# Optimization experiments

Hardware: AMD Instinct MI355X
Metric: run time of the kernel (lower is better)

Reference implementation:

```python
import jax, jax.numpy as jnp
import numpy as np
from jax import lax

STRIDE = 4
RADII = (0.1, 0.2)
NSAMPLES = (16, 32)


def fps(xyz, npoint):
    """Iterative farthest point sampling. xyz: (B,N,3) -> idx (B,npoint) int32."""
    B, N, _ = xyz.shape

    def body(carry, _):
        dists, last = carry  # (B,N), (B,)
        last_pt = jnp.take_along_axis(xyz, last[:, None, None], axis=1)  # (B,1,3)
        d = jnp.sum((xyz - last_pt) ** 2, axis=-1)  # (B,N)
        dists = jnp.minimum(dists, d)
        nxt = jnp.argmax(dists, axis=-1).astype(jnp.int32)
        return (dists, nxt), last

    init = (jnp.full((B, N), 1e10, xyz.dtype), jnp.zeros((B,), jnp.int32))
    _, idxs = lax.scan(body, init, None, length=npoint)
    return jnp.transpose(idxs)  # (B, npoint)


def ball_query(radius, nsample, support_xyz, query_xyz):
    """First-nsample-in-ball neighbor indices, padded with the first valid index.
    Returns idx (B,S,K) int32."""
    N = support_xyz.shape[1]
    d2 = (jnp.sum(query_xyz ** 2, -1, keepdims=True)
          + jnp.sum(support_xyz ** 2, -1)[:, None, :]
          - 2.0 * jnp.einsum('bsd,bnd->bsn', query_xyz, support_xyz))  # (B,S,N)
    in_ball = d2 <= radius * radius
    key = jnp.where(in_ball, jnp.arange(N, dtype=jnp.int32), N)  # smallest index first
    neg_key, idx = lax.top_k(-key, nsample)  # smallest keys
    valid = (-neg_key) < N
    idx = jnp.where(valid, idx, idx[..., :1])  # pad empty slots with first neighbor
    return idx


def gather_points(pts, idx):
    """pts (B,N,D), idx (B,S,K) -> (B,S,K,D)"""
    B, S, K = idx.shape
    D = pts.shape[-1]
    out = jnp.take_along_axis(pts, idx.reshape(B, S * K, 1), axis=1)
    return out.reshape(B, S, K, D)


def scale_block(query_xyz, support_xyz, feats_t, radius, nsample, weights):
    idx = ball_query(radius, nsample, support_xyz, query_xyz)
    g_xyz = gather_points(support_xyz, idx) - query_xyz[:, :, None, :]  # relative coords
    g_feat = gather_points(feats_t, idx)
    h = jnp.concatenate([g_xyz, g_feat], axis=-1)  # (B,S,K,3+C)
    for W, b in weights:  # shared pointwise MLP (1x1 conv) + ReLU
        h = jax.nn.relu(jnp.einsum('bskc,cd->bskd', h, W) + b)
    return jnp.max(h, axis=2)  # max-pool over neighbors -> (B,S,Cout)


def setup_inputs() -> dict:
    key = jax.random.key(0)
    ks = jax.random.split(key, 10)
    B, N, C = 8, 8192, 64
    inp = {
        'support_xyz': jax.random.uniform(ks[0], (B, N, 3), jnp.float32),
        'support_features': jax.random.normal(ks[1], (B, C, N), jnp.float32),
    }
    dims0 = [(67, 64), (64, 64), (64, 128)]
    dims1 = [(67, 64), (64, 96), (96, 128)]
    k = 2
    for s, dims in ((0, dims0), (1, dims1)):
        for j, (din, dout) in enumerate(dims):
            inp[f's{s}_w{j}'] = jax.random.normal(ks[k], (din, dout), jnp.float32) * 0.02
            inp[f's{s}_b{j}'] = jnp.zeros((dout,), jnp.float32)
            k += 1
    return inp


def reference(support_xyz, support_features,
              s0_w0, s0_b0, s0_w1, s0_b1, s0_w2, s0_b2,
              s1_w0, s1_b0, s1_w1, s1_b1, s1_w2, s1_b2):
    B, N, _ = support_xyz.shape
    npoint = N // STRIDE
    idx = fps(support_xyz, npoint)  # (B,npoint)
    query_xyz = jnp.take_along_axis(support_xyz, idx[:, :, None], axis=1)  # (B,npoint,3)
    feats_t = jnp.transpose(support_features, (0, 2, 1))  # (B,N,C)
    w0 = [(s0_w0, s0_b0), (s0_w1, s0_b1), (s0_w2, s0_b2)]
    w1 = [(s1_w0, s1_b0), (s1_w1, s1_b1), (s1_w2, s1_b2)]
    f0 = scale_block(query_xyz, support_xyz, feats_t, RADII[0], NSAMPLES[0], w0)
    f1 = scale_block(query_xyz, support_xyz, feats_t, RADII[1], NSAMPLES[1], w1)
    new_features = jnp.transpose(jnp.concatenate([f0, f1], axis=-1), (0, 2, 1))  # (B,256,npoint)
    return query_xyz, new_features
```

## Files before the change

### kernel.cpp

```cpp
#include <hip/hip_runtime.h>

#define N_SUP 8192
#define N_QPT 2048

typedef float v2f __attribute__((ext_vector_type(2)));

__device__ __forceinline__ float sumsq3(float x, float y, float z) {
#pragma clang fp contract(off)
  return x * x + y * y + z * z;
}

__device__ __forceinline__ float dot3(float ax, float ay, float az,
                                      float bx, float by, float bz) {
#pragma clang fp contract(off)
  return ax * bx + ay * by + az * bz;
}

__device__ __forceinline__ float d2_expand(float A, float Bn, float d) {
#pragma clang fp contract(off)
  return (A + Bn) - 2.0f * d;
}

template <int CTRL>
__device__ __forceinline__ float dppmax(float m) {
  int mi = __float_as_int(m);
  int mv = __builtin_amdgcn_update_dpp(mi, mi, CTRL, 0xf, 0xf, false);
  return fmaxf(m, __int_as_float(mv));
}

__device__ __forceinline__ float wavemax_dpp(float m) {
  m = dppmax<0x111>(m);
  m = dppmax<0x112>(m);
  m = dppmax<0x114>(m);
  m = dppmax<0x118>(m);
  m = dppmax<0x142>(m);
  m = dppmax<0x143>(m);
  return m;
}

template <int CTRL>
__device__ __forceinline__ unsigned dppminu(unsigned m) {
  unsigned mv = (unsigned)__builtin_amdgcn_update_dpp((int)m, (int)m, CTRL,
                                                      0xf, 0xf, false);
  return (mv < m) ? mv : m;
}

__device__ __forceinline__ unsigned wavemin_dpp(unsigned m) {
  m = dppminu<0x111>(m);
  m = dppminu<0x112>(m);
  m = dppminu<0x114>(m);
  m = dppminu<0x118>(m);
  m = dppminu<0x142>(m);
  m = dppminu<0x143>(m);
  return m;
}

__global__ __launch_bounds__(256) void prep_xyz_kernel(
    const float* __restrict__ xyz, float* __restrict__ xs,
    float* __restrict__ ys, float* __restrict__ zs, float* __restrict__ bsq) {
  int p = blockIdx.x * 256 + threadIdx.x;
  float x = xyz[p * 3 + 0];
  float y = xyz[p * 3 + 1];
  float z = xyz[p * 3 + 2];
  xs[p] = x; ys[p] = y; zs[p] = z;
  bsq[p] = sumsq3(x, y, z);
}

__global__ __launch_bounds__(256) void transpose_feats_kernel(
    const float* __restrict__ feats, float* __restrict__ fT) {
  __shared__ float tile[64][65];
  int b = blockIdx.x >> 7;
  int nb = (blockIdx.x & 127) << 6;
  int t = threadIdx.x;
#pragma unroll
  for (int i = 0; i < 16; ++i) {
    int e = i * 256 + t;
    int c = e >> 6, n = e & 63;
    tile[n][c] = feats[(b * 64 + c) * N_SUP + nb + n];
  }
  __syncthreads();
#pragma unroll
  for (int i = 0; i < 16; ++i) {
    int e = i * 256 + t;
    int n = e >> 6, c = e & 63;
    fT[(b * N_SUP + nb + n) * 64 + c] = tile[n][c];
  }
}

__global__ __launch_bounds__(512, 1) void fps_kernel(
    const float* __restrict__ xs, const float* __restrict__ ys,
    const float* __restrict__ zs, float* __restrict__ qxyz) {
  const int b = blockIdx.x;
  const int t = threadIdx.x;
  __shared__ float sx[N_SUP], sy[N_SUP], sz[N_SUP];
  __shared__ __align__(16) unsigned long long skey[2][8];
  const float* bx = xs + b * N_SUP;
  const float* by = ys + b * N_SUP;
  const float* bz = zs + b * N_SUP;
  v2f px[8], py[8], pz[8], dm[8];
#pragma unroll
  for (int j = 0; j < 8; ++j) {
    int n0 = t + (2 * j) * 512, n1 = t + (2 * j + 1) * 512;
    float x0 = bx[n0], x1 = bx[n1];
    float y0 = by[n0], y1 = by[n1];
    float z0 = bz[n0], z1 = bz[n1];
    px[j] = (v2f){x0, x1}; py[j] = (v2f){y0, y1}; pz[j] = (v2f){z0, z1};
    sx[n0] = x0; sx[n1] = x1;
    sy[n0] = y0; sy[n1] = y1;
    sz[n0] = z0; sz[n1] = z1;
    dm[j] = (v2f){1e10f, 1e10f};
  }
  float lx = bx[0], ly = by[0], lz = bz[0];
  float* q = qxyz + b * N_QPT * 3;
  if (t == 0) { q[0] = lx; q[1] = ly; q[2] = lz; }
  const int wv = t >> 6;
  const bool is63 = (t & 63) == 63;
  for (int it = 1; it < N_QPT; ++it) {
    float nx = -lx, ny = -ly, nz = -lz;
    v2f nx2 = (v2f){nx, nx}, ny2 = (v2f){ny, ny}, nz2 = (v2f){nz, nz};
    float lm = -1.0f;
#pragma unroll
    for (int j = 0; j < 8; ++j) {
#pragma clang fp contract(off)
      v2f dx = px[j] + nx2;
      v2f dy = py[j] + ny2;
      v2f dz = pz[j] + nz2;
      v2f s = dx * dx + dy * dy;
      s = s + dz * dz;
      v2f nd = __builtin_elementwise_min(dm[j], s);
      dm[j] = nd;
      lm = fmaxf(lm, fmaxf(nd.x, nd.y));
    }
    float wmx = wavemax_dpp(lm);
    float wm = __int_as_float(
        __builtin_amdgcn_readlane(__float_as_int(wmx), 63));
    int slot = 0x10000;
#pragma unroll
    for (int j = 7; j >= 0; --j) {
      if (dm[j].y == wm) slot = 2 * j + 1;
      if (dm[j].x == wm) slot = 2 * j;
    }
    unsigned li = (unsigned)(slot * 512 + t);
    unsigned wli = wavemin_dpp(li);
    if (is63) {
      skey[it & 1][wv] =
          (((unsigned long long)(unsigned)__float_as_int(wmx)) << 32) |
          (unsigned)(N_SUP - 1 - (int)wli);
    }
    __syncthreads();
    const ulonglong2* pk = (const ulonglong2*)&skey[it & 1][0];
    ulonglong2 A = pk[0], B = pk[1], C = pk[2], D = pk[3];
    unsigned long long k0 = (A.y > A.x) ? A.y : A.x;
    unsigned long long k1 = (B.y > B.x) ? B.y : B.x;
    unsigned long long k2 = (C.y > C.x) ? C.y : C.x;
    unsigned long long k3 = (D.y > D.x) ? D.y : D.x;
    k0 = (k1 > k0) ? k1 : k0;
    k2 = (k3 > k2) ? k3 : k2;
    k0 = (k2 > k0) ? k2 : k0;
    int ri = N_SUP - 1 - (int)(unsigned)(k0 & 0xFFFFFFFFull);
    lx = sx[ri]; ly = sy[ri]; lz = sz[ri];
    if (t == 0) { q[it * 3 + 0] = lx; q[it * 3 + 1] = ly; q[it * 3 + 2] = lz; }
  }
}

__global__ __launch_bounds__(256) void ballquery_kernel(
    const float* __restrict__ qxyz, const float* __restrict__ xs,
    const float* __restrict__ ys, const float* __restrict__ zs,
    const float* __restrict__ bsq, int* __restrict__ idx0,
    int* __restrict__ idx1) {
  const int lane = threadIdx.x & 63;
  const int qg = (blockIdx.x * 256 + threadIdx.x) >> 6;
  const int b = qg >> 11;
  const float qx = qxyz[qg * 3 + 0];
  const float qy = qxyz[qg * 3 + 1];
  const float qz = qxyz[qg * 3 + 2];
  const float A = sumsq3(qx, qy, qz);
  const float* sx = xs + b * N_SUP;
  const float* sy = ys + b * N_SUP;
  const float* sz = zs + b * N_SUP;
  const float* sq = bsq + b * N_SUP;
  int* o0 = idx0 + qg * 16;
  int* o1 = idx1 + qg * 32;
  int cnt0 = 0, cnt1 = 0, first0 = 0, first1 = 0;
  const unsigned long long ltmask = (1ull << lane) - 1ull;
  for (int base = 0; base < N_SUP; base += 64) {
    int n = base + lane;
    float d = dot3(qx, qy, qz, sx[n], sy[n], sz[n]);
    float d2 = d2_expand(A, sq[n], d);
    bool in1 = d2 <= 0.04f;
    bool in0 = d2 <= 0.01f;
    unsigned long long m1 = __ballot(in1);
    unsigned long long m0 = __ballot(in0);
    if (in1) {
      int pos = cnt1 + __popcll(m1 & ltmask);
      if (pos < 32) o1[pos] = n;
    }
    if (in0) {
      int pos = cnt0 + __popcll(m0 & ltmask);
      if (pos < 16) o0[pos] = n;
    }
    if (cnt1 == 0 && m1 != 0ull) first1 = base + __ffsll(m1) - 1;
    if (cnt0 == 0 && m0 != 0ull) first0 = base + __ffsll(m0) - 1;
    cnt1 += __popcll(m1);
    cnt0 += __popcll(m0);
    if (cnt0 >= 16 && cnt1 >= 32) break;
  }
  for (int p = cnt0 + lane; p < 16; p += 64) o0[p] = first0;
  for (int p = cnt1 + lane; p < 32; p += 64) o1[p] = first1;
}

template <int CIN, int SIN, int D, int SOUT>
__device__ __forceinline__ void dense_layer(const float* __restrict__ hin,
                                            float* __restrict__ hout,
                                            const float* __restrict__ W,
                                            const float* __restrict__ Bv,
                                            int w, int lane) {
  constexpr int CH = D / 16;
#pragma unroll
  for (int pass = 0; pass * 4 < CH; ++pass) {
    const int chunk = pass * 4 + w;
    if (chunk < CH) {
      const int co = chunk * 16;
      float acc[16];
#pragma unroll
      for (int j = 0; j < 16; ++j) acc[j] = Bv[co + j];
      const float* hr = hin + lane * SIN;
      const float* wp = W + co;
#pragma unroll 4
      for (int c = 0; c < CIN; ++c) {
        float a = hr[c];
#pragma unroll
        for (int j = 0; j < 16; ++j) acc[j] = fmaf(a, wp[c * D + j], acc[j]);
      }
      float* ho = hout + lane * SOUT + co;
#pragma unroll
      for (int j = 0; j < 16; ++j) ho[j] = fmaxf(acc[j], 0.0f);
    }
  }
}

template <int K, int Q, int C2, int S2, int CHOFF>
__global__ __launch_bounds__(256, 4) void mlp_kernel(
    const int* __restrict__ idxl, const float* __restrict__ qxyz,
    const float* __restrict__ xs, const float* __restrict__ ys,
    const float* __restrict__ zs, const float* __restrict__ fT,
    const float* __restrict__ W1, const float* __restrict__ B1,
    const float* __restrict__ W2, const float* __restrict__ B2,
    const float* __restrict__ W3, const float* __restrict__ B3,
    float* __restrict__ outf) {
  constexpr int S0 = 67, S1 = 65;
  constexpr int H0 = 64 * S0, H1 = 64 * S1, H2 = 64 * S2;
  constexpr int SM = H1 + (H2 > H0 ? H2 : H0);
  __shared__ float smem[SM];
  float* h1 = smem;
  float* h0 = smem + H1;
  float* h2 = smem + H1;
  const int t = threadIdx.x;
  const int w = __builtin_amdgcn_readfirstlane(t >> 6);
  const int lane = t & 63;
  for (int e = t; e < H0; e += 256) {
    int r = e / S0, c = e - r * S0;
    int qi = r / K, k = r - qi * K;
    int qg = blockIdx.x * Q + qi;
    int b = qg >> 11;
    int n = idxl[qg * K + k];
    float v;
    if (c < 3) {
      const float* sp = (c == 0) ? xs : (c == 1) ? ys : zs;
      v = sp[b * N_SUP + n] - qxyz[qg * 3 + c];
    } else {
      v = fT[(b * N_SUP + n) * 64 + (c - 3)];
    }
    h0[e] = v;
  }
  __syncthreads();
  dense_layer<67, S0, 64, S1>(h0, h1, W1, B1, w, lane);
  __syncthreads();
  dense_layer<64, S1, C2, S2>(h1, h2, W2, B2, w, lane);
  __syncthreads();
#pragma unroll
  for (int pass = 0; pass < 2; ++pass) {
    const int co = (pass * 4 + w) * 16;
    float acc[16];
#pragma unroll
    for (int j = 0; j < 16; ++j) acc[j] = B3[co + j];
    const float* hr = h2 + lane * S2;
#pragma unroll 4
    for (int c = 0; c < C2; ++c) {
      float a = hr[c];
#pragma unroll
      for (int j = 0; j < 16; ++j) acc[j] = fmaf(a, W3[c * 128 + co + j], acc[j]);
    }
#pragma unroll
    for (int j = 0; j < 16; ++j) acc[j] = fmaxf(acc[j], 0.0f);
#pragma unroll
    for (int off = K / 2; off >= 1; off >>= 1) {
#pragma unroll
      for (int j = 0; j < 16; ++j)
        acc[j] = fmaxf(acc[j], __shfl_xor(acc[j], off));
    }
    if ((lane & (K - 1)) == 0) {
      int qg = blockIdx.x * Q + (lane / K);
      int b = qg >> 11, s = qg & 2047;
      float* dst = outf + ((b * 256 + CHOFF + co) * 2048 + s);
#pragma unroll
      for (int j = 0; j < 16; ++j) dst[j * 2048] = acc[j];
    }
  }
}

extern "C" void kernel_launch(void* const* d_in, const int* in_sizes, int n_in,
                              void* d_out, int out_size, void* d_ws,
                              size_t ws_size, hipStream_t stream) {
  const float* xyz = (const float*)d_in[0];
  const float* feats = (const float*)d_in[1];
  const float* wt[12];
  for (int i = 0; i < 12; ++i) wt[i] = (const float*)d_in[2 + i];

  float* ws = (float*)d_ws;
  float* xs = ws;
  float* ys = ws + 65536;
  float* zs = ws + 131072;
  float* bsq = ws + 196608;
  float* fT = ws + 262144;
  int* idx0 = (int*)(ws + 4456448);
  int* idx1 = idx0 + 262144;

  float* qxyz = (float*)d_out;
  float* outf = qxyz + 8 * 2048 * 3;

  prep_xyz_kernel<<<dim3(256), dim3(256), 0, stream>>>(xyz, xs, ys, zs, bsq);
  transpose_feats_kernel<<<dim3(1024), dim3(256), 0, stream>>>(feats, fT);
  fps_kernel<<<dim3(8), dim3(512), 0, stream>>>(xs, ys, zs, qxyz);
  ballquery_kernel<<<dim3(4096), dim3(256), 0, stream>>>(qxyz, xs, ys, zs, bsq,
                                                         idx0, idx1);
  mlp_kernel<16, 4, 64, 65, 0><<<dim3(4096), dim3(256), 0, stream>>>(
      idx0, qxyz, xs, ys, zs, fT, wt[0], wt[1], wt[2], wt[3], wt[4], wt[5],
      outf);
  mlp_kernel<32, 2, 96, 97, 128><<<dim3(8192), dim3(256), 0, stream>>>(
      idx1, qxyz, xs, ys, zs, fT, wt[6], wt[7], wt[8], wt[9], wt[10], wt[11],
      outf);
}
```

Baseline: 2.823 ms.

## Spatially bin FPS points and skip threads whose bounding box cannot change

Points are counting-sorted into an 8x8x8 grid in shared memory so each thread owns 16 spatially coherent points with a bounding box. Each FPS iteration, a thread skips its distance update if the new sample is farther from its box than its current max distance, and whole waves skip the reduction when no lane is dirty. Argmax is reduced as a packed 64-bit key carrying the original index for tie-breaking. This adds a sort prologue, 64-bit DPP reductions, and depends on coordinates lying in [0,1) for the binning.

After: 2.893 ms. +2.5%, slower.

```diff
diff --git a/kernel.cpp b/kernel.cpp
--- a/kernel.cpp
+++ b/kernel.cpp
@@ -22,37 +22,24 @@
 }
 
 template <int CTRL>
-__device__ __forceinline__ float dppmax(float m) {
-  int mi = __float_as_int(m);
-  int mv = __builtin_amdgcn_update_dpp(mi, mi, CTRL, 0xf, 0xf, false);
-  return fmaxf(m, __int_as_float(mv));
-}
-
-__device__ __forceinline__ float wavemax_dpp(float m) {
-  m = dppmax<0x111>(m);
-  m = dppmax<0x112>(m);
-  m = dppmax<0x114>(m);
-  m = dppmax<0x118>(m);
-  m = dppmax<0x142>(m);
-  m = dppmax<0x143>(m);
-  return m;
-}
-
-template <int CTRL>
-__device__ __forceinline__ unsigned dppminu(unsigned m) {
-  unsigned mv = (unsigned)__builtin_amdgcn_update_dpp((int)m, (int)m, CTRL,
-                                                      0xf, 0xf, false);
-  return (mv < m) ? mv : m;
-}
-
-__device__ __forceinline__ unsigned wavemin_dpp(unsigned m) {
-  m = dppminu<0x111>(m);
-  m = dppminu<0x112>(m);
-  m = dppminu<0x114>(m);
-  m = dppminu<0x118>(m);
-  m = dppminu<0x142>(m);
-  m = dppminu<0x143>(m);
-  return m;
+__device__ __forceinline__ unsigned long long dppmax64(unsigned long long k) {
+  unsigned lo = (unsigned)k, hi = (unsigned)(k >> 32);
+  unsigned olo =
+      (unsigned)__builtin_amdgcn_update_dpp((int)lo, (int)lo, CTRL, 0xf, 0xf, false);
+  unsigned ohi =
+      (unsigned)__builtin_amdgcn_update_dpp((int)hi, (int)hi, CTRL, 0xf, 0xf, false);
+  unsigned long long o = (((unsigned long long)ohi) << 32) | olo;
+  return (o > k) ? o : k;
+}
+
+__device__ __forceinline__ unsigned long long wavemax_u64(unsigned long long k) {
+  k = dppmax64<0x111>(k);
+  k = dppmax64<0x112>(k);
+  k = dppmax64<0x114>(k);
+  k = dppmax64<0x118>(k);
+  k = dppmax64<0x142>(k);
+  k = dppmax64<0x143>(k);
+  return k;
 }
 
 __global__ __launch_bounds__(256) void prep_xyz_kernel(
@@ -93,60 +80,115 @@
   const int b = blockIdx.x;
   const int t = threadIdx.x;
   __shared__ float sx[N_SUP], sy[N_SUP], sz[N_SUP];
+  __shared__ unsigned short sorig[N_SUP];
+  __shared__ unsigned int hist[512], offs[512], cursor[512];
   __shared__ __align__(16) unsigned long long skey[2][8];
   const float* bx = xs + b * N_SUP;
   const float* by = ys + b * N_SUP;
   const float* bz = zs + b * N_SUP;
+
+  hist[t] = 0u;
+  __syncthreads();
+  for (int j = 0; j < 16; ++j) {
+    int n = t + j * 512;
+    float x = bx[n], y = by[n], z = bz[n];
+    int cx = min(7, (int)(x * 8.0f));
+    int cy = min(7, (int)(y * 8.0f));
+    int cz = min(7, (int)(z * 8.0f));
+    atomicAdd(&hist[(cx << 6) | (cy << 3) | cz], 1u);
+  }
+  __syncthreads();
+  offs[t] = hist[t];
+  __syncthreads();
+  for (int d = 1; d < 512; d <<= 1) {
+    unsigned v = (t >= d) ? offs[t - d] : 0u;
+    __syncthreads();
+    offs[t] += v;
+    __syncthreads();
+  }
+  cursor[t] = offs[t] - hist[t];
+  __syncthreads();
+  for (int j = 0; j < 16; ++j) {
+    int n = t + j * 512;
+    float x = bx[n], y = by[n], z = bz[n];
+    int cx = min(7, (int)(x * 8.0f));
+    int cy = min(7, (int)(y * 8.0f));
+    int cz = min(7, (int)(z * 8.0f));
+    unsigned pos = atomicAdd(&cursor[(cx << 6) | (cy << 3) | cz], 1u);
+    sx[pos] = x; sy[pos] = y; sz[pos] = z;
+    sorig[pos] = (unsigned short)n;
+  }
+  __syncthreads();
+
   v2f px[8], py[8], pz[8], dm[8];
+  unsigned payx[8], payy[8];
+  const int base = t * 16;
 #pragma unroll
   for (int j = 0; j < 8; ++j) {
-    int n0 = t + (2 * j) * 512, n1 = t + (2 * j + 1) * 512;
-    float x0 = bx[n0], x1 = bx[n1];
-    float y0 = by[n0], y1 = by[n1];
-    float z0 = bz[n0], z1 = bz[n1];
-    px[j] = (v2f){x0, x1}; py[j] = (v2f){y0, y1}; pz[j] = (v2f){z0, z1};
-    sx[n0] = x0; sx[n1] = x1;
-    sy[n0] = y0; sy[n1] = y1;
-    sz[n0] = z0; sz[n1] = z1;
+    int p0 = base + 2 * j, p1 = p0 + 1;
+    px[j] = (v2f){sx[p0], sx[p1]};
+    py[j] = (v2f){sy[p0], sy[p1]};
+    pz[j] = (v2f){sz[p0], sz[p1]};
+    payx[j] = ((unsigned)(N_SUP - 1 - sorig[p0]) << 13) | (unsigned)p0;
+    payy[j] = ((unsigned)(N_SUP - 1 - sorig[p1]) << 13) | (unsigned)p1;
     dm[j] = (v2f){1e10f, 1e10f};
   }
-  float lx = bx[0], ly = by[0], lz = bz[0];
+  float lox = px[0].x, hix = px[0].x;
+  float loy = py[0].x, hiy = py[0].x;
+  float loz = pz[0].x, hiz = pz[0].x;
+#pragma unroll
+  for (int j = 0; j < 8; ++j) {
+    lox = fminf(lox, fminf(px[j].x, px[j].y));
+    hix = fmaxf(hix, fmaxf(px[j].x, px[j].y));
+    loy = fminf(loy, fminf(py[j].x, py[j].y));
+    hiy = fmaxf(hiy, fmaxf(py[j].x, py[j].y));
+    loz = fminf(loz, fminf(pz[j].x, pz[j].y));
+    hiz = fmaxf(hiz, fmaxf(pz[j].x, pz[j].y));
+  }
+  float tval = 1e10f;
+  unsigned long long tkey = 0ull, wkey = 0ull;
+
+  float lxp = bx[0], lyp = by[0], lzp = bz[0];
   float* q = qxyz + b * N_QPT * 3;
-  if (t == 0) { q[0] = lx; q[1] = ly; q[2] = lz; }
+  if (t == 0) { q[0] = lxp; q[1] = lyp; q[2] = lzp; }
   const int wv = t >> 6;
   const bool is63 = (t & 63) == 63;
+
   for (int it = 1; it < N_QPT; ++it) {
-    float nx = -lx, ny = -ly, nz = -lz;
-    v2f nx2 = (v2f){nx, nx}, ny2 = (v2f){ny, ny}, nz2 = (v2f){nz, nz};
-    float lm = -1.0f;
-#pragma unroll
-    for (int j = 0; j < 8; ++j) {
+    float dxl = fmaxf(fmaxf(lox - lxp, lxp - hix), 0.0f);
+    float dyl = fmaxf(fmaxf(loy - lyp, lyp - hiy), 0.0f);
+    float dzl = fmaxf(fmaxf(loz - lzp, lzp - hiz), 0.0f);
+    float db2 = dxl * dxl + dyl * dyl + dzl * dzl;
+    bool dirty = db2 < tval * 1.0001f + 1e-12f;
+    if (__ballot(dirty)) {
+      if (dirty) {
+        float nx = -lxp, ny = -lyp, nz = -lzp;
+        v2f nx2 = (v2f){nx, nx}, ny2 = (v2f){ny, ny}, nz2 = (v2f){nz, nz};
+        float lm = -1.0f;
+#pragma unroll
+        for (int j = 0; j < 8; ++j) {
 #pragma clang fp contract(off)
-      v2f dx = px[j] + nx2;
-      v2f dy = py[j] + ny2;
-      v2f dz = pz[j] + nz2;
-      v2f s = dx * dx + dy * dy;
-      s = s + dz * dz;
-      v2f nd = __builtin_elementwise_min(dm[j], s);
-      dm[j] = nd;
-      lm = fmaxf(lm, fmaxf(nd.x, nd.y));
-    }
-    float wmx = wavemax_dpp(lm);
-    float wm = __int_as_float(
-        __builtin_amdgcn_readlane(__float_as_int(wmx), 63));
-    int slot = 0x10000;
-#pragma unroll
-    for (int j = 7; j >= 0; --j) {
-      if (dm[j].y == wm) slot = 2 * j + 1;
-      if (dm[j].x == wm) slot = 2 * j;
-    }
-    unsigned li = (unsigned)(slot * 512 + t);
-    unsigned wli = wavemin_dpp(li);
-    if (is63) {
-      skey[it & 1][wv] =
-          (((unsigned long long)(unsigned)__float_as_int(wmx)) << 32) |
-          (unsigned)(N_SUP - 1 - (int)wli);
-    }
+          v2f dx = px[j] + nx2;
+          v2f dy = py[j] + ny2;
+          v2f dz = pz[j] + nz2;
+          v2f s = dx * dx + dy * dy;
+          s = s + dz * dz;
+          v2f nd = __builtin_elementwise_min(dm[j], s);
+          dm[j] = nd;
+          lm = fmaxf(lm, fmaxf(nd.x, nd.y));
+        }
+        tval = lm;
+        unsigned pay = 0u;
+#pragma unroll
+        for (int j = 0; j < 8; ++j) {
+          if (dm[j].x == tval) pay = max(pay, payx[j]);
+          if (dm[j].y == tval) pay = max(pay, payy[j]);
+        }
+        tkey = (((unsigned long long)__float_as_uint(tval)) << 32) | pay;
+      }
+      wkey = wavemax_u64(tkey);
+    }
+    if (is63) skey[it & 1][wv] = wkey;
     __syncthreads();
     const ulonglong2* pk = (const ulonglong2*)&skey[it & 1][0];
     ulonglong2 A = pk[0], B = pk[1], C = pk[2], D = pk[3];
@@ -157,9 +199,9 @@
     k0 = (k1 > k0) ? k1 : k0;
     k2 = (k3 > k2) ? k3 : k2;
     k0 = (k2 > k0) ? k2 : k0;
-    int ri = N_SUP - 1 - (int)(unsigned)(k0 & 0xFFFFFFFFull);
-    lx = sx[ri]; ly = sy[ri]; lz = sz[ri];
-    if (t == 0) { q[it * 3 + 0] = lx; q[it * 3 + 1] = ly; q[it * 3 + 2] = lz; }
+    unsigned pos = (unsigned)k0 & 0x1FFFu;
+    lxp = sx[pos]; lyp = sy[pos]; lzp = sz[pos];
+    if (t == 0) { q[it * 3 + 0] = lxp; q[it * 3 + 1] = lyp; q[it * 3 + 2] = lzp; }
   }
 }
 
```
